# Kernel optimization log

Measured on AMD Instinct MI355X. Metric: run time of the kernel, lower is better.

## Reference

```python
import jax, jax.numpy as jnp
import numpy as np

HEADS = 6
WSIZE = 8
SHIFTS = 4
EPS = 1e-5


def conv1x1(x, w, b=None):
    # x: (B,C,H,W), w: (O,C)
    y = jnp.einsum('bchw,oc->bohw', x, w)
    if b is not None:
        y = y + b[None, :, None, None]
    return y


def spatial_shift(x):
    # ShiftConv2d1 depthwise fixed-kernel conv == per-group spatial shift with zero pad
    C = x.shape[1]
    g = C // 5
    x0, x1, x2, x3, x4 = (x[:, :g], x[:, g:2 * g], x[:, 2 * g:3 * g],
                          x[:, 3 * g:4 * g], x[:, 4 * g:])
    left = jnp.pad(x0[:, :, :, 1:], ((0, 0), (0, 0), (0, 0), (0, 1)))   # kernel (1,2)
    right = jnp.pad(x1[:, :, :, :-1], ((0, 0), (0, 0), (0, 0), (1, 0)))  # kernel (1,0)
    up = jnp.pad(x2[:, :, 1:, :], ((0, 0), (0, 0), (0, 1), (0, 0)))      # kernel (2,1)
    down = jnp.pad(x3[:, :, :-1, :], ((0, 0), (0, 0), (1, 0), (0, 0)))   # kernel (0,1)
    return jnp.concatenate([left, right, up, down, x4], axis=1)


def window_attn(xb, ws, heads, shifts):
    # xb: (B, 2*heads*c, H, W); self-similarity attention q@q^T (no separate K, no scaling)
    if shifts > 0:
        xb = jnp.roll(xb, (-(ws // 2), -(ws // 2)), axis=(2, 3))
    b, c2, H, W = xb.shape
    cd = c2 // (2 * heads)
    nh, nw = H // ws, W // ws
    t = xb.reshape(b, 2, heads, cd, nh, ws, nw, ws)
    t = t.transpose(1, 0, 4, 6, 2, 5, 7, 3).reshape(2, b * nh * nw, heads, ws * ws, cd)
    q, v = t[0], t[1]
    atn = jax.nn.softmax(jnp.einsum('whnc,whmc->whnm', q, q), axis=-1)
    o = jnp.einsum('whnm,whmc->whnc', atn, v)
    o = o.reshape(b, nh, nw, heads, ws, ws, cd)
    o = o.transpose(0, 3, 6, 1, 4, 2, 5).reshape(b, heads * cd, H, W)
    if shifts > 0:
        o = jnp.roll(o, (ws // 2, ws // 2), axis=(2, 3))
    return o


def setup_inputs() -> dict:
    key = jax.random.key(0)
    ks = jax.random.split(key, 8)
    B, C, H, W = 2, 180, 256, 256
    s = 0.05
    return {
        'x': jax.random.normal(ks[0], (B, C, H, W), jnp.float32),
        'w0': jax.random.normal(ks[1], (2 * C, C), jnp.float32) * s,
        'b0': jnp.zeros((2 * C,), jnp.float32),
        'w1': jax.random.normal(ks[2], (C, 2 * C), jnp.float32) * s,
        'b1': jnp.zeros((C,), jnp.float32),
        'w_in': jax.random.normal(ks[3], (2 * C, C), jnp.float32) * s,
        'b_in': jnp.zeros((2 * C,), jnp.float32),
        'bn_g': jnp.ones((2 * C,), jnp.float32),
        'bn_b': jnp.zeros((2 * C,), jnp.float32),
        'w_out': jax.random.normal(ks[4], (C, C), jnp.float32) * s,
        'b_out': jnp.zeros((C,), jnp.float32),
    }


def reference(x, w0, b0, w1, b1, w_in, b_in, bn_g, bn_b, w_out, b_out):
    # --- LFE (shift-conv FFN), exp_ratio=2, relu ---
    y = conv1x1(spatial_shift(x), w0, b0)
    y = jax.nn.relu(y)
    y = conv1x1(spatial_shift(y), w1, b1)
    x = y + x
    # --- GMSA (3 parallel shifted-window self-similarity attentions) ---
    z = conv1x1(x, w_in, b_in)
    mu = z.mean(axis=(0, 2, 3), keepdims=True)
    var = z.var(axis=(0, 2, 3), keepdims=True)  # biased, matching BN training forward
    z = (z - mu) / jnp.sqrt(var + EPS) * bn_g[None, :, None, None] + bn_b[None, :, None, None]
    cs = z.shape[1] // 3
    sizes = [WSIZE // 4, WSIZE // 2, WSIZE]
    outs = [window_attn(z[:, i * cs:(i + 1) * cs], sizes[i], HEADS, SHIFTS)
            for i in range(3)]
    out = conv1x1(jnp.concatenate(outs, axis=1), w_out, b_out)
    return out + x
```

## Files before the change

### kernel.cpp

```cpp
#include <hip/hip_runtime.h>
#include <hip/hip_bf16.h>

#define HWSZ 65536
#define NPIX 131072

typedef unsigned short u16;
typedef __bf16 bf16x8 __attribute__((ext_vector_type(8)));
typedef float f32x4 __attribute__((ext_vector_type(4)));
typedef unsigned short u16x2 __attribute__((ext_vector_type(2)));
typedef unsigned short u16x4 __attribute__((ext_vector_type(4)));
typedef unsigned short u16x8 __attribute__((ext_vector_type(8)));
typedef unsigned short u16x8u __attribute__((ext_vector_type(8), aligned(4)));

__device__ inline u16 f2bf(float f) {
    unsigned int x = __builtin_bit_cast(unsigned int, f);
    unsigned int r = x + 0x7FFFu + ((x >> 16) & 1u);
    return (u16)(r >> 16);
}
__device__ inline float bf2f(u16 u) {
    unsigned int x = ((unsigned int)u) << 16;
    return __builtin_bit_cast(float, x);
}

__global__ __launch_bounds__(256) void prep_w(
    const float* __restrict__ w0, const float* __restrict__ w1,
    const float* __restrict__ wi, const float* __restrict__ wo,
    u16* __restrict__ W0p, u16* __restrict__ W1p,
    u16* __restrict__ Wip, u16* __restrict__ Wop)
{
    const int i = blockIdx.x * 256 + threadIdx.x;
    {
        const int r = i / 192, c = i % 192;
        const bool ok = (r < 360) && (c < 180);
        W0p[i] = ok ? f2bf(w0[r * 180 + c]) : (u16)0;
        Wip[i] = ok ? f2bf(wi[r * 180 + c]) : (u16)0;
    }
    {
        const int r = i / 384, c = i % 384;
        W1p[i] = (r < 180 && c < 360) ? f2bf(w1[r * 360 + c]) : (u16)0;
    }
    if (i < 36864) {
        const int r = i / 192, c = i % 192;
        Wop[i] = (r < 180 && c < 180) ? f2bf(wo[r * 180 + c]) : (u16)0;
    }
}

template<int CI, int G, int INM, int XSTR, bool RELU>
__global__ __launch_bounds__(512) void conv_v14(
    const void* __restrict__ Xv, const u16* __restrict__ Wp,
    const float* __restrict__ bias, u16* __restrict__ Yh)
{
    constexpr int CI_PAD = ((CI + 31) / 32) * 32;
    constexpr int NSTEP  = CI_PAD / 32;
    constexpr int LDK    = 40;

    __shared__ u16 Xt[2][64 * LDK];

    const int tid = threadIdx.x;
    const int p0   = blockIdx.x << 6;
    const int b    = p0 >> 16;
    const int pix0 = p0 & 65535;
    const int h    = pix0 >> 8;
    const int w0c  = pix0 & 255;
    const int lane = tid & 63, wid = tid >> 6;
    const int lr = lane & 15, lg = lane >> 4;
    const int co_wave = wid * 48;

    const float* Xf = (const float*)Xv + (size_t)b * CI * HWSZ;
    const u16*   Xh = (const u16*)Xv;

    const int xn  = tid & 63;
    const int k4a = tid >> 6;

    auto loadX = [&](int kt, u16x4& r) {
        const int c0 = kt + k4a * 4;
        u16x4 v = {0, 0, 0, 0};
        if (c0 < CI) {
            int dh = 0, dw = 0;
            if (G > 0) {
                const int g = c0 / G;
                if      (g == 0) dw = 1;
                else if (g == 1) dw = -1;
                else if (g == 2) dh = 1;
                else if (g == 3) dh = -1;
            }
            const int hh = h + dh;
            const int wp = w0c + xn + dw;
            if (hh >= 0 && hh < 256 && wp >= 0 && wp < 256) {
                if constexpr (INM == 1) {
                    v = *(const u16x4*)&Xh[(size_t)((b << 16) | (hh << 8) | wp) * XSTR + c0];
                } else {
                    const float* xs = Xf + (size_t)c0 * HWSZ + hh * 256 + wp;
                    #pragma unroll
                    for (int j = 0; j < 4; ++j) v[j] = f2bf(xs[(size_t)j * HWSZ]);
                }
            }
        }
        r = v;
    };

    auto loadW = [&](int kt, bf16x8 (&a)[3]) {
        #pragma unroll
        for (int mf = 0; mf < 3; ++mf)
            a[mf] = *(const bf16x8*)&Wp[(size_t)(co_wave + mf * 16 + lr) * CI_PAD + kt + lg * 8];
    };

    auto writeLDS = [&](u16x4& r, int buf) {
        *(u16x4*)&Xt[buf][xn * LDK + k4a * 4] = r;
    };

    f32x4 acc[3][4] = {};
    u16x4 raw[2];
    bf16x8 af[2][3];

    loadX(0, raw[0]);
    loadW(0, af[0]);
    writeLDS(raw[0], 0);

    #pragma unroll
    for (int s = 0; s < NSTEP; ++s) {
        const int cur = s & 1, nxt = cur ^ 1;
        __syncthreads();
        if (s + 1 < NSTEP) {
            loadX((s + 1) * 32, raw[nxt]);
            loadW((s + 1) * 32, af[nxt]);
        }
        bf16x8 bfr[4];
        #pragma unroll
        for (int nf = 0; nf < 4; ++nf)
            bfr[nf] = *(const bf16x8*)&Xt[cur][(nf * 16 + lr) * LDK + lg * 8];
        #pragma unroll
        for (int mf = 0; mf < 3; ++mf)
            #pragma unroll
            for (int nf = 0; nf < 4; ++nf)
                acc[mf][nf] = __builtin_amdgcn_mfma_f32_16x16x32_bf16(
                    af[cur][mf], bfr[nf], acc[mf][nf], 0, 0, 0);
        if (s + 1 < NSTEP) writeLDS(raw[nxt], nxt);
    }

    #pragma unroll
    for (int mf = 0; mf < 3; ++mf) {
        const int co_b = co_wave + mf * 16 + lg * 4;
        if (co_b >= 360) continue;
        #pragma unroll
        for (int nf = 0; nf < 4; ++nf) {
            const size_t pg = (size_t)p0 + nf * 16 + lr;
            u16x4 o;
            #pragma unroll
            for (int r = 0; r < 4; ++r) {
                float v = acc[mf][nf][r] + bias[co_b + r];
                if (RELU) v = fmaxf(v, 0.f);
                o[r] = f2bf(v);
            }
            *(u16x4*)&Yh[pg * 360 + co_b] = o;
        }
    }
}

template<int CI, int CO, int G, int XSTR, bool RELU, int RES, int OUTM, int OSTR, bool COSPLIT>
__global__ __launch_bounds__(256) void conv_v10(
    const u16* __restrict__ Xh, const u16* __restrict__ Wp,
    const float* __restrict__ bias, const void* __restrict__ Rv,
    void* __restrict__ Yv)
{
    constexpr int CI_PAD = ((CI + 31) / 32) * 32;
    constexpr int NSTEP  = CI_PAD / 32;

    __shared__ u16 Xt[2][256 * 8];

    const int tid = threadIdx.x;
    const int bid = blockIdx.x;
    int px_tile, co0;
    if (COSPLIT) {
        co0     = ((bid >> 3) & 1) * 192;
        px_tile = ((bid >> 4) << 3) | (bid & 7);
    } else {
        co0 = blockIdx.y * 192; px_tile = bid;
    }
    const int p0   = px_tile << 6;
    const int b    = p0 >> 16;
    const int pix0 = p0 & 65535;
    const int h    = pix0 >> 8;
    const int w0c  = pix0 & 255;
    const int lane = tid & 63, wid = tid >> 6;
    const int lr = lane & 15, lg = lane >> 4;
    const int co_wave = co0 + wid * 48;

    const int sg  = (wid << 6) | lane;
    const int spx = sg >> 2;
    const int khp = sg & 3;
    const int kh  = khp ^ ((spx >> 1) & 3);

    auto stage = [&](int kt, int buf) {
        const int c0 = kt + kh * 8;
        u16* ldst_lane = &Xt[buf][sg * 8];
        int dh = 0, dw = 0; bool uni = true;
        if (G > 0) {
            const int g0 = c0 / G;
            uni = (g0 == (c0 + 7) / G);
            if      (g0 == 0) dw = 1;
            else if (g0 == 1) dw = -1;
            else if (g0 == 2) dh = 1;
            else if (g0 == 3) dh = -1;
        }
        const int hh = h + dh, wp = w0c + spx + dw;
        const bool pxok = (hh >= 0 && hh < 256 && wp >= 0 && wp < 256);
        if (c0 < CI && uni && pxok) {
            const u16* src = &Xh[(size_t)((b << 16) | (hh << 8) | wp) * XSTR + c0];
            u16* wbase = &Xt[buf][(wid << 6) * 8];
            __builtin_amdgcn_global_load_lds(
                (const __attribute__((address_space(1))) unsigned int*)src,
                (__attribute__((address_space(3))) unsigned int*)wbase, 16, 0, 0);
        } else {
            u16x8 t = {0, 0, 0, 0, 0, 0, 0, 0};
            if (c0 < CI && pxok) {
                #pragma unroll
                for (int j = 0; j < 8; ++j) {
                    const int c = c0 + j;
                    if (c < CI) {
                        int dh2 = 0, dw2 = 0;
                        if (G > 0) {
                            const int g = c / G;
                            if      (g == 0) dw2 = 1;
                            else if (g == 1) dw2 = -1;
                            else if (g == 2) dh2 = 1;
                            else if (g == 3) dh2 = -1;
                        }
                        const int h2 = h + dh2, w2 = w0c + spx + dw2;
                        if (h2 >= 0 && h2 < 256 && w2 >= 0 && w2 < 256)
                            t[j] = Xh[(size_t)((b << 16) | (h2 << 8) | w2) * XSTR + c];
                    }
                }
            }
            *(u16x8*)ldst_lane = t;
        }
    };

    auto loadW = [&](int kt, bf16x8 (&a)[3]) {
        #pragma unroll
        for (int mf = 0; mf < 3; ++mf)
            a[mf] = *(const bf16x8*)&Wp[(size_t)(co_wave + mf * 16 + lr) * CI_PAD + kt + lg * 8];
    };

    f32x4 acc[3][4] = {};
    bf16x8 af[2][3];

    stage(0, 0);
    loadW(0, af[0]);
    __syncthreads();

    #pragma unroll
    for (int s = 0; s < NSTEP; ++s) {
        const int cur = s & 1, nxt = cur ^ 1;
        if (s + 1 < NSTEP) {
            stage((s + 1) * 32, nxt);
            loadW((s + 1) * 32, af[nxt]);
        }
        bf16x8 bfr[4];
        #pragma unroll
        for (int nf = 0; nf < 4; ++nf) {
            const int pxr = nf * 16 + lr;
            const int kpp = lg ^ ((pxr >> 1) & 3);
            bfr[nf] = *(const bf16x8*)&Xt[cur][pxr * 32 + kpp * 8];
        }
        #pragma unroll
        for (int mf = 0; mf < 3; ++mf)
            #pragma unroll
            for (int nf = 0; nf < 4; ++nf)
                acc[mf][nf] = __builtin_amdgcn_mfma_f32_16x16x32_bf16(
                    af[cur][mf], bfr[nf], acc[mf][nf], 0, 0, 0);
        __syncthreads();
    }

    const float* Rf = (const float*)Rv;
    const u16*   Rh = (const u16*)Rv;
    #pragma unroll
    for (int mf = 0; mf < 3; ++mf) {
        const int co_b = co_wave + mf * 16 + lg * 4;
        if (co_b >= CO) continue;
        #pragma unroll
        for (int nf = 0; nf < 4; ++nf) {
            const int pl = pix0 + nf * 16 + lr;
            const size_t pg = (size_t)p0 + nf * 16 + lr;
            float v[4];
            #pragma unroll
            for (int r = 0; r < 4; ++r) {
                v[r] = acc[mf][nf][r] + bias[co_b + r];
                if (RELU) v[r] = fmaxf(v[r], 0.f);
            }
            if (RES == 1) {
                #pragma unroll
                for (int r = 0; r < 4; ++r)
                    v[r] += Rf[((size_t)(b * CO + co_b + r)) * HWSZ + pl];
            }
            if (RES == 2) {
                u16x4 rr = *(const u16x4*)&Rh[pg * 180 + co_b];
                #pragma unroll
                for (int r = 0; r < 4; ++r) v[r] += bf2f(rr[r]);
            }
            if (OUTM == 1) {
                u16x4 o;
                #pragma unroll
                for (int r = 0; r < 4; ++r) o[r] = f2bf(v[r]);
                *(u16x4*)&((u16*)Yv)[pg * OSTR + co_b] = o;
            } else {
                #pragma unroll
                for (int r = 0; r < 4; ++r)
                    ((float*)Yv)[((size_t)(b * CO + co_b + r)) * HWSZ + pl] = v[r];
            }
        }
    }
}

__global__ __launch_bounds__(256) void bn_part(const u16* __restrict__ zt,
                                               float* __restrict__ part)
{
    const int tid = threadIdx.x;
    const int oc  = tid & 63;
    const int pp  = tid >> 6;
    if (oc >= 45) return;
    const int stripe = blockIdx.x * 4 + pp;
    const int pb = blockIdx.x * 1024 + pp;
    float s[8] = {}, q[8] = {};
    for (int i = 0; i < 256; ++i) {
        const int p = pb + i * 4;
        u16x8 t = *(const u16x8*)&zt[(size_t)p * 360 + oc * 8];
        #pragma unroll
        for (int j = 0; j < 8; ++j) {
            float v = bf2f(t[j]);
            s[j] += v; q[j] += v * v;
        }
    }
    float* pr = part + ((size_t)stripe * 45 + oc) * 16;
    #pragma unroll
    for (int j = 0; j < 8; ++j) { pr[j] = s[j]; pr[8 + j] = q[j]; }
}

__global__ __launch_bounds__(256) void bn_fin(const float* __restrict__ part,
                                              const float* __restrict__ g,
                                              const float* __restrict__ bb,
                                              float* __restrict__ sc,
                                              float* __restrict__ sh)
{
    const int oc = blockIdx.x;
    const int t  = threadIdx.x;
    const float* p1 = part + ((size_t)t * 45 + oc) * 16;
    const float* p2 = part + ((size_t)(t + 256) * 45 + oc) * 16;
    float v[16];
    #pragma unroll
    for (int k = 0; k < 16; ++k) v[k] = p1[k] + p2[k];
    #pragma unroll
    for (int k = 0; k < 16; ++k)
        for (int m = 32; m; m >>= 1) v[k] += __shfl_xor(v[k], m, 64);
    __shared__ float red[4][16];
    if ((t & 63) == 0) {
        #pragma unroll
        for (int k = 0; k < 16; ++k) red[t >> 6][k] = v[k];
    }
    __syncthreads();
    if (t == 0) {
        const float invN = 1.f / (float)NPIX;
        #pragma unroll
        for (int j = 0; j < 8; ++j) {
            const int c = oc * 8 + j;
            float su = red[0][j] + red[1][j] + red[2][j] + red[3][j];
            float sq = red[0][8+j] + red[1][8+j] + red[2][8+j] + red[3][8+j];
            float mean = su * invN;
            float var  = sq * invN - mean * mean;
            float istd = 1.f / sqrtf(var + 1e-5f);
            float s = g[c] * istd;
            sc[c] = s;
            sh[c] = bb[c] - mean * s;
        }
    }
}

template<int WS>
__global__ __launch_bounds__(256) void attn_v3(
    const u16* __restrict__ zt, const float* __restrict__ scale,
    const float* __restrict__ shiftc, u16* __restrict__ ot, int chunk)
{
    constexpr int NP  = WS * WS;
    constexpr int GPB = 256 / NP;
    constexpr int SH  = WS / 2;
    constexpr int NW  = 256 / WS;

    __shared__ float qs[256 * 12];
    __shared__ float vs[256 * 12];
    __shared__ float scs[120], shs[120];

    const int tid = threadIdx.x;
    if (tid < 120) {
        scs[tid] = scale[chunk * 120 + tid];
        shs[tid] = shiftc[chunk * 120 + tid];
    }

    const int lg  = tid / NP;
    const int n   = tid % NP;
    const int gidx = blockIdx.x * GPB + lg;

    const int head = gidx % 6;
    const int win  = gidx / 6;
    const int wcol = win % NW;
    const int tmp  = win / NW;
    const int wrow = tmp % NW;
    const int b    = tmp / NW;

    const int i = n / WS, j = n % WS;
    const int hh = (wrow * WS + i + SH) & 255;
    const int ww = (wcol * WS + j + SH) & 255;
    const size_t zrow = (size_t)((b << 16) | (hh << 8) | ww) * 360;

    const int cq = chunk * 120 + head * 10;
    const int cl = head * 10;

    u16x8u q8 = *(const u16x8u*)&zt[zrow + cq];
    u16x2  q2 = *(const u16x2*)&zt[zrow + cq + 8];
    u16x8u v8 = *(const u16x8u*)&zt[zrow + cq + 60];
    u16x2  v2 = *(const u16x2*)&zt[zrow + cq + 68];
    __syncthreads();

    float q[10];
    float* qrow = &qs[tid * 12];
    float* vrow = &vs[tid * 12];
    #pragma unroll
    for (int c = 0; c < 8; ++c) {
        q[c] = bf2f(q8[c]) * scs[cl + c] + shs[cl + c];
        qrow[c] = q[c];
        vrow[c] = bf2f(v8[c]) * scs[60 + cl + c] + shs[60 + cl + c];
    }
    q[8] = bf2f(q2[0]) * scs[cl + 8] + shs[cl + 8];
    q[9] = bf2f(q2[1]) * scs[cl + 9] + shs[cl + 9];
    qrow[8] = q[8]; qrow[9] = q[9];
    vrow[8] = bf2f(v2[0]) * scs[60 + cl + 8] + shs[60 + cl + 8];
    vrow[9] = bf2f(v2[1]) * scs[60 + cl + 9] + shs[60 + cl + 9];
    qrow[10] = 0.f; qrow[11] = 0.f;
    vrow[10] = 0.f; vrow[11] = 0.f;
    __syncthreads();

    const float* qg = &qs[(lg * NP) * 12];
    const float* vg = &vs[(lg * NP) * 12];

    float mx = -1e30f;
    for (int m = 0; m < NP; ++m) {
        f32x4 a0 = *(const f32x4*)&qg[m * 12];
        f32x4 a1 = *(const f32x4*)&qg[m * 12 + 4];
        f32x4 a2 = *(const f32x4*)&qg[m * 12 + 8];
        float d = q[0]*a0[0] + q[1]*a0[1] + q[2]*a0[2] + q[3]*a0[3]
                + q[4]*a1[0] + q[5]*a1[1] + q[6]*a1[2] + q[7]*a1[3]
                + q[8]*a2[0] + q[9]*a2[1];
        mx = fmaxf(mx, d);
    }
    float s = 0.f;
    float o[10] = {};
    for (int m = 0; m < NP; ++m) {
        f32x4 a0 = *(const f32x4*)&qg[m * 12];
        f32x4 a1 = *(const f32x4*)&qg[m * 12 + 4];
        f32x4 a2 = *(const f32x4*)&qg[m * 12 + 8];
        float d = q[0]*a0[0] + q[1]*a0[1] + q[2]*a0[2] + q[3]*a0[3]
                + q[4]*a1[0] + q[5]*a1[1] + q[6]*a1[2] + q[7]*a1[3]
                + q[8]*a2[0] + q[9]*a2[1];
        float e = __expf(d - mx);
        s += e;
        f32x4 b0 = *(const f32x4*)&vg[m * 12];
        f32x4 b1 = *(const f32x4*)&vg[m * 12 + 4];
        f32x4 b2 = *(const f32x4*)&vg[m * 12 + 8];
        o[0] += e * b0[0]; o[1] += e * b0[1]; o[2] += e * b0[2]; o[3] += e * b0[3];
        o[4] += e * b1[0]; o[5] += e * b1[1]; o[6] += e * b1[2]; o[7] += e * b1[3];
        o[8] += e * b2[0]; o[9] += e * b2[1];
    }
    const float inv = 1.f / s;
    u16* orow = ot + (size_t)((b << 16) | (hh << 8) | ww) * 180 + chunk * 60 + head * 10;
    u16x8u o8;
    #pragma unroll
    for (int c = 0; c < 8; ++c) o8[c] = f2bf(o[c] * inv);
    u16x2 o2;
    o2[0] = f2bf(o[8] * inv);
    o2[1] = f2bf(o[9] * inv);
    *(u16x8u*)&orow[0] = o8;
    *(u16x2*)&orow[8]  = o2;
}

extern "C" void kernel_launch(void* const* d_in, const int* in_sizes, int n_in,
                              void* d_out, int out_size, void* d_ws, size_t ws_size,
                              hipStream_t stream)
{
    const float* x     = (const float*)d_in[0];
    const float* w0    = (const float*)d_in[1];
    const float* b0    = (const float*)d_in[2];
    const float* w1    = (const float*)d_in[3];
    const float* b1    = (const float*)d_in[4];
    const float* w_in  = (const float*)d_in[5];
    const float* b_in  = (const float*)d_in[6];
    const float* bn_g  = (const float*)d_in[7];
    const float* bn_b  = (const float*)d_in[8];
    const float* w_out = (const float*)d_in[9];
    const float* b_out = (const float*)d_in[10];
    float* out = (float*)d_out;

    u16* y   = (u16*)d_ws;
    u16* x1b = y   + (size_t)NPIX * 360;
    u16* ot  = x1b + (size_t)NPIX * 180;
    u16* W0p = ot  + (size_t)NPIX * 180;
    u16* Wip = W0p + 384 * 192;
    u16* W1p = Wip + 384 * 192;
    u16* Wop = W1p + 192 * 384;
    float* part   = (float*)(Wop + 192 * 192);
    float* scale  = part + 512 * 45 * 16;
    float* shiftc = scale + 360;
    u16* zt = y;

    dim3 blk(256);
    dim3 blk8(512);

    prep_w<<<dim3(288), blk, 0, stream>>>(w0, w1, w_in, w_out, W0p, W1p, Wip, Wop);

    conv_v14<180, 36, 0, 0,   true >
        <<<dim3(2048), blk8, 0, stream>>>(x, W0p, b0, y);
    conv_v10<360, 180, 72, 360, false, 1, 1, 180, false>
        <<<dim3(2048, 1), blk, 0, stream>>>(y, W1p, b1, x, x1b);
    conv_v14<180, 0,  1, 180, false>
        <<<dim3(2048), blk8, 0, stream>>>(x1b, Wip, b_in, zt);
    bn_part<<<dim3(128), blk, 0, stream>>>(zt, part);
    bn_fin<<<dim3(45), blk, 0, stream>>>(part, bn_g, bn_b, scale, shiftc);
    attn_v3<2><<<dim3(3072), blk, 0, stream>>>(zt, scale, shiftc, ot, 0);
    attn_v3<4><<<dim3(3072), blk, 0, stream>>>(zt, scale, shiftc, ot, 1);
    attn_v3<8><<<dim3(3072), blk, 0, stream>>>(zt, scale, shiftc, ot, 2);
    conv_v10<180, 180, 0,  180, false, 2, 0, 0, false>
        <<<dim3(2048, 1), blk, 0, stream>>>(ot, Wop, b_out, x1b, out);
}
```

Baseline: 398.5 us.

## Fuse batch-norm partial statistics into the input-projection conv epilogue

The input 1x1 conv now accumulates per-channel sums and sums of squares of its bf16-rounded outputs in registers, reduces them across lanes with shuffles, and writes one partial per block. This removes the separate bn_part pass that re-read the whole 131072x360 bf16 z tensor, and a new bn_fin2 reduces the 2048 per-block partials for each channel. In exchange the conv epilogue does extra shuffle and store work, and the final reduction reads a larger partial buffer with a strided access pattern.

```diff
diff --git a/kernel.cpp b/kernel.cpp
--- a/kernel.cpp
+++ b/kernel.cpp
@@ -45,10 +45,11 @@
     }
 }
 
-template<int CI, int G, int INM, int XSTR, bool RELU>
+template<int CI, int G, int INM, int XSTR, bool RELU, bool BNPART>
 __global__ __launch_bounds__(512) void conv_v14(
     const void* __restrict__ Xv, const u16* __restrict__ Wp,
-    const float* __restrict__ bias, u16* __restrict__ Yh)
+    const float* __restrict__ bias, u16* __restrict__ Yh,
+    float* __restrict__ part)
 {
     constexpr int CI_PAD = ((CI + 31) / 32) * 32;
     constexpr int NSTEP  = CI_PAD / 32;
@@ -138,6 +139,7 @@
         if (s + 1 < NSTEP) writeLDS(raw[nxt], nxt);
     }
 
+    float bsum[3][4] = {}, bsq[3][4] = {};
     #pragma unroll
     for (int mf = 0; mf < 3; ++mf) {
         const int co_b = co_wave + mf * 16 + lg * 4;
@@ -151,9 +153,73 @@
                 float v = acc[mf][nf][r] + bias[co_b + r];
                 if (RELU) v = fmaxf(v, 0.f);
                 o[r] = f2bf(v);
+                if (BNPART) {
+                    const float vr = bf2f(o[r]);
+                    bsum[mf][r] += vr;
+                    bsq[mf][r]  += vr * vr;
+                }
             }
             *(u16x4*)&Yh[pg * 360 + co_b] = o;
         }
+    }
+
+    if (BNPART) {
+        #pragma unroll
+        for (int mf = 0; mf < 3; ++mf)
+            #pragma unroll
+            for (int r = 0; r < 4; ++r) {
+                #pragma unroll
+                for (int m = 1; m < 16; m <<= 1) {
+                    bsum[mf][r] += __shfl_xor(bsum[mf][r], m, 64);
+                    bsq[mf][r]  += __shfl_xor(bsq[mf][r],  m, 64);
+                }
+            }
+        if (lr == 0) {
+            float* pb = part + (size_t)blockIdx.x * 768;
+            #pragma unroll
+            for (int mf = 0; mf < 3; ++mf) {
+                const int co_b = co_wave + mf * 16 + lg * 4;
+                if (co_b >= 360) continue;
+                f32x4 s4, q4;
+                #pragma unroll
+                for (int r = 0; r < 4; ++r) { s4[r] = bsum[mf][r]; q4[r] = bsq[mf][r]; }
+                *(f32x4*)&pb[co_b]       = s4;
+                *(f32x4*)&pb[384 + co_b] = q4;
+            }
+        }
+    }
+}
+
+__global__ __launch_bounds__(256) void bn_fin2(const float* __restrict__ part,
+                                               const float* __restrict__ g,
+                                               const float* __restrict__ bb,
+                                               float* __restrict__ sc,
+                                               float* __restrict__ sh)
+{
+    const int c = blockIdx.x;
+    const int t = threadIdx.x;
+    float s = 0.f, q = 0.f;
+    for (int k = t; k < 2048; k += 256) {
+        s += part[(size_t)k * 768 + c];
+        q += part[(size_t)k * 768 + 384 + c];
+    }
+    for (int m = 32; m; m >>= 1) {
+        s += __shfl_xor(s, m, 64);
+        q += __shfl_xor(q, m, 64);
+    }
+    __shared__ float rs[4], rq[4];
+    if ((t & 63) == 0) { rs[t >> 6] = s; rq[t >> 6] = q; }
+    __syncthreads();
+    if (t == 0) {
+        const float su = rs[0] + rs[1] + rs[2] + rs[3];
+        const float sq = rq[0] + rq[1] + rq[2] + rq[3];
+        const float invN = 1.f / (float)NPIX;
+        const float mean = su * invN;
+        const float var  = sq * invN - mean * mean;
+        const float istd = 1.f / sqrtf(var + 1e-5f);
+        const float scv  = g[c] * istd;
+        sc[c] = scv;
+        sh[c] = bb[c] - mean * scv;
     }
 }
 
@@ -308,69 +374,6 @@
                 for (int r = 0; r < 4; ++r)
                     ((float*)Yv)[((size_t)(b * CO + co_b + r)) * HWSZ + pl] = v[r];
             }
-        }
-    }
-}
-
-__global__ __launch_bounds__(256) void bn_part(const u16* __restrict__ zt,
-                                               float* __restrict__ part)
-{
-    const int tid = threadIdx.x;
-    const int oc  = tid & 63;
-    const int pp  = tid >> 6;
-    if (oc >= 45) return;
-    const int stripe = blockIdx.x * 4 + pp;
-    const int pb = blockIdx.x * 1024 + pp;
-    float s[8] = {}, q[8] = {};
-    for (int i = 0; i < 256; ++i) {
-        const int p = pb + i * 4;
-        u16x8 t = *(const u16x8*)&zt[(size_t)p * 360 + oc * 8];
-        #pragma unroll
-        for (int j = 0; j < 8; ++j) {
-            float v = bf2f(t[j]);
-            s[j] += v; q[j] += v * v;
-        }
-    }
-    float* pr = part + ((size_t)stripe * 45 + oc) * 16;
-    #pragma unroll
-    for (int j = 0; j < 8; ++j) { pr[j] = s[j]; pr[8 + j] = q[j]; }
-}
-
-__global__ __launch_bounds__(256) void bn_fin(const float* __restrict__ part,
-                                              const float* __restrict__ g,
-                                              const float* __restrict__ bb,
-                                              float* __restrict__ sc,
-                                              float* __restrict__ sh)
-{
-    const int oc = blockIdx.x;
-    const int t  = threadIdx.x;
-    const float* p1 = part + ((size_t)t * 45 + oc) * 16;
-    const float* p2 = part + ((size_t)(t + 256) * 45 + oc) * 16;
-    float v[16];
-    #pragma unroll
-    for (int k = 0; k < 16; ++k) v[k] = p1[k] + p2[k];
-    #pragma unroll
-    for (int k = 0; k < 16; ++k)
-        for (int m = 32; m; m >>= 1) v[k] += __shfl_xor(v[k], m, 64);
-    __shared__ float red[4][16];
-    if ((t & 63) == 0) {
-        #pragma unroll
-        for (int k = 0; k < 16; ++k) red[t >> 6][k] = v[k];
-    }
-    __syncthreads();
-    if (t == 0) {
-        const float invN = 1.f / (float)NPIX;
-        #pragma unroll
-        for (int j = 0; j < 8; ++j) {
-            const int c = oc * 8 + j;
-            float su = red[0][j] + red[1][j] + red[2][j] + red[3][j];
-            float sq = red[0][8+j] + red[1][8+j] + red[2][8+j] + red[3][8+j];
-            float mean = su * invN;
-            float var  = sq * invN - mean * mean;
-            float istd = 1.f / sqrtf(var + 1e-5f);
-            float s = g[c] * istd;
-            sc[c] = s;
-            sh[c] = bb[c] - mean * s;
         }
     }
 }
@@ -506,7 +509,7 @@
     u16* W1p = Wip + 384 * 192;
     u16* Wop = W1p + 192 * 384;
     float* part   = (float*)(Wop + 192 * 192);
-    float* scale  = part + 512 * 45 * 16;
+    float* scale  = part + (size_t)2048 * 768;
     float* shiftc = scale + 360;
     u16* zt = y;
 
@@ -515,14 +518,13 @@
 
     prep_w<<<dim3(288), blk, 0, stream>>>(w0, w1, w_in, w_out, W0p, W1p, Wip, Wop);
 
-    conv_v14<180, 36, 0, 0,   true >
-        <<<dim3(2048), blk8, 0, stream>>>(x, W0p, b0, y);
+    conv_v14<180, 36, 0, 0,   true,  false>
+        <<<dim3(2048), blk8, 0, stream>>>(x, W0p, b0, y, nullptr);
     conv_v10<360, 180, 72, 360, false, 1, 1, 180, false>
         <<<dim3(2048, 1), blk, 0, stream>>>(y, W1p, b1, x, x1b);
-    conv_v14<180, 0,  1, 180, false>
-        <<<dim3(2048), blk8, 0, stream>>>(x1b, Wip, b_in, zt);
-    bn_part<<<dim3(128), blk, 0, stream>>>(zt, part);
-    bn_fin<<<dim3(45), blk, 0, stream>>>(part, bn_g, bn_b, scale, shiftc);
+    conv_v14<180, 0,  1, 180, false, true >
+        <<<dim3(2048), blk8, 0, stream>>>(x1b, Wip, b_in, zt, part);
+    bn_fin2<<<dim3(360), blk, 0, stream>>>(part, bn_g, bn_b, scale, shiftc);
     attn_v3<2><<<dim3(3072), blk, 0, stream>>>(zt, scale, shiftc, ot, 0);
     attn_v3<4><<<dim3(3072), blk, 0, stream>>>(zt, scale, shiftc, ot, 1);
     attn_v3<8><<<dim3(3072), blk, 0, stream>>>(zt, scale, shiftc, ot, 2);
```

Measured after the change: 387.0 us, median of 3. 2.9% less time.
